# Performance work log

Measured on AMD Instinct MI355X. Metric: run time of the kernel, lower is better.

Reference implementation:

```python
import jax, jax.numpy as jnp
import numpy as np

N_NODES = 50000  # 4 node types x 12500
N_PER = 12500
E = 600000
H = 128
IN_DIMS = [128, 128, 64, 64]


def setup_inputs() -> dict:
    key = jax.random.key(0)
    ks = jax.random.split(key, 16)
    inp = {}
    for i, d in enumerate(IN_DIMS):
        inp[f"feat{i}"] = jax.random.normal(ks[i], (N_PER, d), dtype=jnp.float32)
        # xavier_normal-ish init, gain 1.414
        std = 1.414 * np.sqrt(2.0 / (d + H))
        inp[f"W_fc{i}"] = jax.random.normal(ks[4 + i], (d, H), dtype=jnp.float32) * std
        inp[f"b_fc{i}"] = jnp.zeros((H,), dtype=jnp.float32)
    inp["src"] = jax.random.randint(ks[8], (E,), 0, N_NODES, dtype=jnp.int32)
    inp["dst"] = jax.random.randint(ks[9], (E,), 0, N_NODES, dtype=jnp.int32)
    inp["e_feat"] = jax.random.randint(ks[10], (E,), 0, 36, dtype=jnp.int32)
    inp["b_g0"] = jnp.zeros((H,), dtype=jnp.float32)  # GraphConv layer0 (weight=False, bias)
    inp["W_g1"] = jax.random.normal(ks[11], (H, H), dtype=jnp.float32) * np.sqrt(1.0 / H)
    inp["b_g1"] = jnp.zeros((H,), dtype=jnp.float32)
    return inp


def _degree_norms(src, dst):
    ones = jnp.ones((src.shape[0],), dtype=jnp.float32)
    deg_out = jax.ops.segment_sum(ones, src, num_segments=N_NODES)
    deg_in = jax.ops.segment_sum(ones, dst, num_segments=N_NODES)
    # DGL norm='both': D_out^{-1/2} on src side, D_in^{-1/2} on dst side (clamp 0-degree)
    out_norm = jax.lax.rsqrt(jnp.maximum(deg_out, 1.0))
    in_norm = jax.lax.rsqrt(jnp.maximum(deg_in, 1.0))
    return out_norm, in_norm


def _gcn_aggregate(h, src, dst, out_norm, in_norm):
    m = (h * out_norm[:, None])[src]                      # [E, H] gather
    agg = jax.ops.segment_sum(m, dst, num_segments=N_NODES)
    return agg * in_norm[:, None]


def reference(feat0, feat1, feat2, feat3,
              W_fc0, b_fc0, W_fc1, b_fc1, W_fc2, b_fc2, W_fc3, b_fc3,
              src, dst, e_feat, b_g0, W_g1, b_g1):
    # per-node-type linear projections, then concat along node dim
    h = jnp.concatenate([
        feat0 @ W_fc0 + b_fc0,
        feat1 @ W_fc1 + b_fc1,
        feat2 @ W_fc2 + b_fc2,
        feat3 @ W_fc3 + b_fc3,
    ], axis=0)  # [N_NODES, H]

    out_norm, in_norm = _degree_norms(src, dst)
    # GraphConv layer 0: weight=False, bias, activation (dropout p=0 -> identity)
    h = jax.nn.relu(_gcn_aggregate(h, src, dst, out_norm, in_norm) + b_g0)
    # GraphConv layer 1: aggregate, then linear weight + bias, activation
    h = jax.nn.relu(_gcn_aggregate(h, src, dst, out_norm, in_norm) @ W_g1 + b_g1)

    e = e_feat.astype(jnp.float32)  # e_feat.reshape(-1,1).float() in original
    # forward graph: msg = ft + sum_{r in 0..4} where(e==r, ft, 0) = ft * (1 + 1{e in 0..4})
    w_fwd = 1.0 + sum((e == float(r)).astype(jnp.float32) for r in (0, 1, 2, 3, 4))
    agg_a = jax.ops.segment_sum(h[src] * w_fwd[:, None], dst, num_segments=N_NODES)
    # transpose graph (reversed edges, same e): msg = sum_{r in {6,14,30}} where(e==r, ft, 0)
    w_bwd = sum((e == float(r)).astype(jnp.float32) for r in (6, 14, 30))
    agg_b = jax.ops.segment_sum(h[dst] * w_bwd[:, None], src, num_segments=N_NODES)
    return agg_a + agg_b
```

## Files before the change

### kernel.cpp

```cpp
#include <hip/hip_runtime.h>
#include <hip/hip_bf16.h>

#define N_NODES 50000
#define N_PER   12500
#define E_EDGES 600000
#define HDIM    128

#define NBLK_FC    ((N_PER + 63) / 64)
#define NBLK_NODE  ((N_NODES + 255) / 256)
#define MASK31  0x7fffffff

#define HQD 64
#define HSL_D (E_EDGES / HQD)
#define NBLK_DB (HQD * 4)
#define HQS 32
#define HSL_S (E_EDGES / HQS)
#define NBLK_S (HQS * 4)

typedef __attribute__((ext_vector_type(8))) short bfrag;
typedef __attribute__((ext_vector_type(4))) float ffrag;

__device__ __forceinline__ unsigned short f2bf(float f) {
    union { float f; unsigned u; } x; x.f = f;
    unsigned r = x.u + 0x7fffu + ((x.u >> 16) & 1u);
    return (unsigned short)(r >> 16);
}
__device__ __forceinline__ float lo_bf(unsigned v) { return __uint_as_float(v << 16); }
__device__ __forceinline__ float hi_bf(unsigned v) { return __uint_as_float(v & 0xffff0000u); }
__device__ __forceinline__ unsigned pack2(float a, float b) {
    return (unsigned)f2bf(a) | ((unsigned)f2bf(b) << 16);
}
__device__ __forceinline__ float onrm_of(int deg) {
    return rsqrtf(fmaxf((float)deg, 1.0f));
}

__device__ __forceinline__ void acc8_add(float* acc, uint4 v) {
    acc[0] += lo_bf(v.x); acc[1] += hi_bf(v.x);
    acc[2] += lo_bf(v.y); acc[3] += hi_bf(v.y);
    acc[4] += lo_bf(v.z); acc[5] += hi_bf(v.z);
    acc[6] += lo_bf(v.w); acc[7] += hi_bf(v.w);
}
__device__ __forceinline__ void acc8_addw(float* acc, uint4 v, float w) {
    acc[0] += lo_bf(v.x) * w; acc[1] += hi_bf(v.x) * w;
    acc[2] += lo_bf(v.y) * w; acc[3] += hi_bf(v.y) * w;
    acc[4] += lo_bf(v.z) * w; acc[5] += hi_bf(v.z) * w;
    acc[6] += lo_bf(v.w) * w; acc[7] += hi_bf(v.w) * w;
}

__global__ __launch_bounds__(256) void prep_kernel(
    const float* __restrict__ W0, const float* __restrict__ W1,
    const float* __restrict__ W2, const float* __restrict__ W3,
    const float* __restrict__ Wg,
    const int* __restrict__ src, const int* __restrict__ dst,
    const int* __restrict__ ef,
    unsigned short* __restrict__ Wp,
    unsigned short* __restrict__ partialS,
    unsigned short* __restrict__ partialD,
    unsigned char*  __restrict__ partialB) {
    __shared__ unsigned hist[N_PER];
    int b = blockIdx.x;
    if (b < NBLK_DB) {
        const int q = b >> 2;
        const int p = b & 3;
        const int g0 = p * N_PER;
        for (int j = threadIdx.x; j < N_PER; j += 256) hist[j] = 0;
        __syncthreads();
        const int e0 = q * HSL_D;
        for (int i = e0 + threadIdx.x; i < e0 + HSL_D; i += 256) {
            int d = dst[i], t = ef[i], s = src[i];
            unsigned rd = (unsigned)(d - g0);
            if (rd < (unsigned)N_PER) atomicAdd(&hist[rd], 1u);
            if (t == 6 || t == 14 || t == 30) {
                unsigned rs = (unsigned)(s - g0);
                if (rs < (unsigned)N_PER) atomicAdd(&hist[rs], 0x10000u);
            }
        }
        __syncthreads();
        for (int j = threadIdx.x; j < N_PER; j += 256) {
            unsigned h = hist[j];
            partialD[(size_t)q * N_NODES + g0 + j] = (unsigned short)(h & 0xffffu);
            partialB[(size_t)q * N_NODES + g0 + j] = (unsigned char)(h >> 16);
        }
    } else if (b < NBLK_DB + NBLK_S) {
        const int r = b - NBLK_DB;
        const int q = r >> 2;
        const int p = r & 3;
        const int g0 = p * N_PER;
        for (int j = threadIdx.x; j < N_PER; j += 256) hist[j] = 0;
        __syncthreads();
        const int e0 = q * HSL_S;
        for (int i = e0 + threadIdx.x; i < e0 + HSL_S; i += 256) {
            unsigned rr = (unsigned)(src[i] - g0);
            if (rr < (unsigned)N_PER) atomicAdd(&hist[rr], 1u);
        }
        __syncthreads();
        for (int j = threadIdx.x; j < N_PER; j += 256)
            partialS[(size_t)q * N_NODES + g0 + j] = (unsigned short)hist[j];
    } else {
        int tid = (b - (NBLK_DB + NBLK_S)) * 256 + threadIdx.x;
        const float* W; int D, base, off;
        if      (tid < 2048) { W = W0; D = 128; base = 0;    off = 0;     }
        else if (tid < 4096) { W = W1; D = 128; base = 2048; off = 16384; }
        else if (tid < 5120) { W = W2; D = 64;  base = 4096; off = 32768; }
        else if (tid < 6144) { W = W3; D = 64;  base = 5120; off = 40960; }
        else                 { W = Wg; D = 128; base = 6144; off = 49152; }
        int t2 = tid - base;
        int KT = D / 32;
        int l = t2 & 63;
        int tt = t2 >> 6;
        int kt = tt % KT, n0 = tt / KT;
        int n = n0 * 16 + (l & 15);
        int kb = kt * 32 + (l >> 4) * 8;
#pragma unroll
        for (int j = 0; j < 8; ++j)
            Wp[(size_t)off + (size_t)t2 * 8 + j] = f2bf(W[(size_t)(kb + j) * 128 + n]);
    }
}

__global__ __launch_bounds__(256) void plane_prefix_kernel(
    unsigned short* __restrict__ partialD, unsigned char* __restrict__ partialB,
    int* __restrict__ degD, int* __restrict__ degB,
    int* __restrict__ scanD, int* __restrict__ scanB,
    int* __restrict__ blocksumD, int* __restrict__ blocksumB) {
    const int t = threadIdx.x;
    const int n = blockIdx.x * 256 + t;
    int dD = 0, dB = 0;
    if (n < N_NODES) {
        int run = 0;
#pragma unroll
        for (int q = 0; q < HQD; ++q) {
            size_t ix = (size_t)q * N_NODES + n;
            int c = partialD[ix];
            partialD[ix] = (unsigned short)run;
            run += c;
        }
        dD = run; degD[n] = run;
        run = 0;
#pragma unroll
        for (int q = 0; q < HQD; ++q) {
            size_t ix = (size_t)q * N_NODES + n;
            int c = partialB[ix];
            partialB[ix] = (unsigned char)run;
            run += c;
        }
        dB = run; degB[n] = run;
    }
    __shared__ int sD[256], sB[256];
    sD[t] = dD; sB[t] = dB;
    __syncthreads();
    for (int off = 1; off < 256; off <<= 1) {
        int xD = (t >= off) ? sD[t - off] : 0;
        int xB = (t >= off) ? sB[t - off] : 0;
        __syncthreads();
        sD[t] += xD; sB[t] += xB;
        __syncthreads();
    }
    if (n < N_NODES) {
        scanD[n] = sD[t] - dD;
        scanB[n] = sB[t] - dB;
    }
    if (t == 255) {
        blocksumD[blockIdx.x] = sD[255];
        blocksumB[blockIdx.x] = sB[255];
    }
}

__global__ __launch_bounds__(256) void base_add_kernel(
    const int* __restrict__ blocksumD, const int* __restrict__ blocksumB,
    int* __restrict__ scanD, int* __restrict__ scanB) {
    __shared__ int sD[256], sB[256];
    const int t = threadIdx.x;
    const int bid = blockIdx.x;
    sD[t] = (t < bid) ? blocksumD[t] : 0;
    sB[t] = (t < bid) ? blocksumB[t] : 0;
    __syncthreads();
    for (int off = 128; off >= 1; off >>= 1) {
        if (t < off) { sD[t] += sD[t + off]; sB[t] += sB[t + off]; }
        __syncthreads();
    }
    const int n = bid * 256 + t;
    if (n < N_NODES) { scanD[n] += sD[0]; scanB[n] += sB[0]; }
}

__global__ __launch_bounds__(1024) void scatter_kernel(
    const int* __restrict__ src, const int* __restrict__ dst,
    const int* __restrict__ ef,
    const unsigned short* __restrict__ prefD,
    const unsigned char*  __restrict__ prefB,
    const int* __restrict__ scanD, const int* __restrict__ scanB,
    int* __restrict__ bucket, int* __restrict__ bucketB)
{
    __shared__ unsigned offP[N_PER];
    const int b = blockIdx.x;
    const int q = b >> 2;
    const int p = b & 3;
    const int g0 = p * N_PER;
    for (int j = threadIdx.x; j < N_PER; j += 1024)
        offP[j] = (unsigned)(scanD[g0 + j] + (int)prefD[(size_t)q * N_NODES + g0 + j])
                | ((unsigned)prefB[(size_t)q * N_NODES + g0 + j] << 20);
    __syncthreads();
    const int e0 = q * HSL_D;
    for (int i = e0 + threadIdx.x; i < e0 + HSL_D; i += 1024) {
        int s = src[i], d = dst[i], t = ef[i];
        unsigned rd = (unsigned)(d - g0);
        if (rd < (unsigned)N_PER) {
            unsigned old = atomicAdd(&offP[rd], 1u);
            bucket[old & 0xFFFFFu] = s | ((t <= 4) ? 0x80000000 : 0);
        }
        if (t == 6 || t == 14 || t == 30) {
            unsigned rs = (unsigned)(s - g0);
            if (rs < (unsigned)N_PER) {
                unsigned old = atomicAdd(&offP[rs], 1u << 20);
                bucketB[scanB[s] + (int)(old >> 20)] = d;
            }
        }
    }
}

template<int D>
__device__ __forceinline__ void fc_body(
    int blk, int tid,
    const float* __restrict__ X,
    const unsigned short* __restrict__ Wp,
    const float* __restrict__ bias,
    unsigned short* __restrict__ outbf,
    int rows)
{
    constexpr int KT = D / 32;
    const int lane = tid & 63;
    const int wave = tid >> 6;
    const int m = lane & 15, q = lane >> 4;
    const int rbase = blk * 64 + wave * 16;
    const int row = rbase + m;

    bfrag afr[KT];
#pragma unroll
    for (int kt = 0; kt < KT; ++kt) {
        bfrag a;
        if (row < rows) {
            const float* xp = X + (size_t)row * D + kt * 32 + q * 8;
            float4 u0 = *(const float4*)xp;
            float4 u1 = *(const float4*)(xp + 4);
            a[0] = (short)f2bf(u0.x); a[1] = (short)f2bf(u0.y);
            a[2] = (short)f2bf(u0.z); a[3] = (short)f2bf(u0.w);
            a[4] = (short)f2bf(u1.x); a[5] = (short)f2bf(u1.y);
            a[6] = (short)f2bf(u1.z); a[7] = (short)f2bf(u1.w);
        } else {
#pragma unroll
            for (int t = 0; t < 8; ++t) a[t] = 0;
        }
        afr[kt] = a;
    }

    ffrag acc[8];
#pragma unroll
    for (int n0 = 0; n0 < 8; ++n0)
#pragma unroll
        for (int t = 0; t < 4; ++t) acc[n0][t] = 0.f;

#pragma unroll
    for (int n0 = 0; n0 < 8; ++n0)
#pragma unroll
        for (int kt = 0; kt < KT; ++kt) {
            bfrag bfr = *(const bfrag*)(Wp + ((size_t)(n0 * KT + kt) * 64 + lane) * 8);
            acc[n0] = __builtin_amdgcn_mfma_f32_16x16x32_bf16(afr[kt], bfr, acc[n0], 0, 0, 0);
        }

#pragma unroll
    for (int n0 = 0; n0 < 8; ++n0) {
        const int col = n0 * 16 + m;
        const float bj = bias[col];
#pragma unroll
        for (int r = 0; r < 4; ++r) {
            int orow = rbase + q * 4 + r;
            if (orow < rows)
                outbf[(size_t)orow * 128 + col] = f2bf(acc[n0][r] + bj);
        }
    }
}

__global__ __launch_bounds__(256) void fc_kernel(
    const float* __restrict__ f0, const float* __restrict__ f1,
    const float* __restrict__ f2, const float* __restrict__ f3,
    const unsigned short* __restrict__ Wp,
    const float* __restrict__ b0, const float* __restrict__ b1,
    const float* __restrict__ b2, const float* __restrict__ b3,
    unsigned short* __restrict__ Abf)
{
    int fb = blockIdx.x;
    int which = fb / NBLK_FC;
    int blk = fb - which * NBLK_FC;
    if (which == 0)
        fc_body<128>(blk, threadIdx.x, f0, Wp,         b0, Abf + (size_t)0 * N_PER * HDIM, N_PER);
    else if (which == 1)
        fc_body<128>(blk, threadIdx.x, f1, Wp + 16384, b1, Abf + (size_t)1 * N_PER * HDIM, N_PER);
    else if (which == 2)
        fc_body<64>(blk, threadIdx.x, f2, Wp + 32768, b2, Abf + (size_t)2 * N_PER * HDIM, N_PER);
    else
        fc_body<64>(blk, threadIdx.x, f3, Wp + 40960, b3, Abf + (size_t)3 * N_PER * HDIM, N_PER);
}

__global__ __launch_bounds__(256) void scale_kernel(
    uint4* __restrict__ A, const unsigned short* __restrict__ partialS,
    float* __restrict__ onrm_buf) {
    int idx = blockIdx.x * blockDim.x + threadIdx.x;
    int n = idx >> 4, j8 = idx & 15;
    int d = (int)partialS[(size_t)j8 * N_NODES + n]
          + (int)partialS[(size_t)(j8 + 16) * N_NODES + n];
    d += __shfl_xor(d, 1);
    d += __shfl_xor(d, 2);
    d += __shfl_xor(d, 4);
    d += __shfl_xor(d, 8);
    float on = onrm_of(d);
    if (j8 == 0) onrm_buf[n] = on;
    uint4 v = A[(size_t)n * 16 + j8];
    uint4 o;
    o.x = pack2(lo_bf(v.x) * on, hi_bf(v.x) * on);
    o.y = pack2(lo_bf(v.y) * on, hi_bf(v.y) * on);
    o.z = pack2(lo_bf(v.z) * on, hi_bf(v.z) * on);
    o.w = pack2(lo_bf(v.w) * on, hi_bf(v.w) * on);
    A[(size_t)n * 16 + j8] = o;
}

__global__ __launch_bounds__(256) void agg0_kernel(
    const uint4* __restrict__ A,
    const int* __restrict__ bucket, const int* __restrict__ scanD,
    const int* __restrict__ degD,
    const float* __restrict__ onrm_buf, const float* __restrict__ b_g0,
    uint4* __restrict__ B) {
    int idx = blockIdx.x * blockDim.x + threadIdx.x;
    int n = idx >> 4, j8 = idx & 15;
    const int cnt = degD[n];
    const int* bk = bucket + scanD[n];
    float acc[8] = {0.f, 0.f, 0.f, 0.f, 0.f, 0.f, 0.f, 0.f};
    int i = 0;
    for (; i + 4 <= cnt; i += 4) {
        int s0 = bk[i] & MASK31,     s1 = bk[i + 1] & MASK31;
        int s2 = bk[i + 2] & MASK31, s3 = bk[i + 3] & MASK31;
        uint4 v0 = A[(size_t)s0 * 16 + j8];
        uint4 v1 = A[(size_t)s1 * 16 + j8];
        uint4 v2 = A[(size_t)s2 * 16 + j8];
        uint4 v3 = A[(size_t)s3 * 16 + j8];
        acc8_add(acc, v0); acc8_add(acc, v1);
        acc8_add(acc, v2); acc8_add(acc, v3);
    }
    for (; i < cnt; ++i) {
        int s = bk[i] & MASK31;
        acc8_add(acc, A[(size_t)s * 16 + j8]);
    }
    float inr = onrm_of(cnt);
    float onr = onrm_buf[n];
    const float* bg = b_g0 + j8 * 8;
    float r[8];
#pragma unroll
    for (int k = 0; k < 8; ++k)
        r[k] = fmaxf(acc[k] * inr + bg[k], 0.f) * onr;
    uint4 o;
    o.x = pack2(r[0], r[1]); o.y = pack2(r[2], r[3]);
    o.z = pack2(r[4], r[5]); o.w = pack2(r[6], r[7]);
    B[(size_t)n * 16 + j8] = o;
}

__global__ __launch_bounds__(256) void gemm1_fused_kernel(
    const unsigned short* __restrict__ Bbf,
    const int* __restrict__ bucket, const int* __restrict__ scanD,
    const int* __restrict__ degD,
    const unsigned short* __restrict__ Wp, const float* __restrict__ bias,
    unsigned short* __restrict__ outbf)
{
    const int lane = threadIdx.x & 63;
    const int wave = threadIdx.x >> 6;
    const int m = lane & 15, q = lane >> 4;
    const int rbase = blockIdx.x * 64 + wave * 16;
    const int node = rbase + m;

    float ga[32];
#pragma unroll
    for (int i = 0; i < 32; ++i) ga[i] = 0.f;

    if (node < N_NODES) {
        const int cnt = degD[node];
        const int* bk = bucket + scanD[node];
        int i = 0;
        for (; i + 2 <= cnt; i += 2) {
            int s0 = bk[i] & MASK31, s1 = bk[i + 1] & MASK31;
            const uint4* r0 = (const uint4*)(Bbf + (size_t)s0 * 128);
            const uint4* r1 = (const uint4*)(Bbf + (size_t)s1 * 128);
            uint4 a0 = r0[0 * 4 + q], a1 = r0[1 * 4 + q], a2 = r0[2 * 4 + q], a3 = r0[3 * 4 + q];
            uint4 c0 = r1[0 * 4 + q], c1 = r1[1 * 4 + q], c2 = r1[2 * 4 + q], c3 = r1[3 * 4 + q];
            acc8_add(ga +  0, a0); acc8_add(ga +  8, a1);
            acc8_add(ga + 16, a2); acc8_add(ga + 24, a3);
            acc8_add(ga +  0, c0); acc8_add(ga +  8, c1);
            acc8_add(ga + 16, c2); acc8_add(ga + 24, c3);
        }
        for (; i < cnt; ++i) {
            int s = bk[i] & MASK31;
            const uint4* rp = (const uint4*)(Bbf + (size_t)s * 128);
#pragma unroll
            for (int kt = 0; kt < 4; ++kt) acc8_add(ga + kt * 8, rp[kt * 4 + q]);
        }
    }

    bfrag afr[4];
#pragma unroll
    for (int kt = 0; kt < 4; ++kt)
#pragma unroll
        for (int j = 0; j < 8; ++j)
            afr[kt][j] = (short)f2bf(ga[kt * 8 + j]);

    ffrag acc[8];
#pragma unroll
    for (int n0 = 0; n0 < 8; ++n0)
#pragma unroll
        for (int t = 0; t < 4; ++t) acc[n0][t] = 0.f;

#pragma unroll
    for (int n0 = 0; n0 < 8; ++n0)
#pragma unroll
        for (int kt = 0; kt < 4; ++kt) {
            bfrag bfr = *(const bfrag*)(Wp + ((size_t)(n0 * 4 + kt) * 64 + lane) * 8);
            acc[n0] = __builtin_amdgcn_mfma_f32_16x16x32_bf16(afr[kt], bfr, acc[n0], 0, 0, 0);
        }

    float ir[4];
#pragma unroll
    for (int r = 0; r < 4; ++r) {
        int orow = rbase + q * 4 + r;
        ir[r] = (orow < N_NODES) ? onrm_of(degD[orow]) : 0.f;
    }
#pragma unroll
    for (int n0 = 0; n0 < 8; ++n0) {
        const int col = n0 * 16 + m;
        const float bj = bias[col];
#pragma unroll
        for (int r = 0; r < 4; ++r) {
            int orow = rbase + q * 4 + r;
            if (orow < N_NODES)
                outbf[(size_t)orow * 128 + col] = f2bf(fmaxf(acc[n0][r] * ir[r] + bj, 0.f));
        }
    }
}

__global__ __launch_bounds__(256) void final_kernel(
    const uint4* __restrict__ H,
    const int* __restrict__ bucket, const int* __restrict__ scanD,
    const int* __restrict__ degD,
    const int* __restrict__ bucketB, const int* __restrict__ scanB,
    const int* __restrict__ degB,
    float4* __restrict__ out4) {
    int idx = blockIdx.x * blockDim.x + threadIdx.x;
    int n = idx >> 4, j8 = idx & 15;
    float acc[8] = {0.f, 0.f, 0.f, 0.f, 0.f, 0.f, 0.f, 0.f};
    const int cnt = degD[n];
    const int* bk = bucket + scanD[n];
    int i = 0;
    for (; i + 4 <= cnt; i += 4) {
        int c0 = bk[i], c1 = bk[i + 1], c2 = bk[i + 2], c3 = bk[i + 3];
        uint4 v0 = H[(size_t)(c0 & MASK31) * 16 + j8];
        uint4 v1 = H[(size_t)(c1 & MASK31) * 16 + j8];
        uint4 v2 = H[(size_t)(c2 & MASK31) * 16 + j8];
        uint4 v3 = H[(size_t)(c3 & MASK31) * 16 + j8];
        acc8_addw(acc, v0, (c0 < 0) ? 2.0f : 1.0f);
        acc8_addw(acc, v1, (c1 < 0) ? 2.0f : 1.0f);
        acc8_addw(acc, v2, (c2 < 0) ? 2.0f : 1.0f);
        acc8_addw(acc, v3, (c3 < 0) ? 2.0f : 1.0f);
    }
    for (; i < cnt; ++i) {
        int c = bk[i];
        acc8_addw(acc, H[(size_t)(c & MASK31) * 16 + j8], (c < 0) ? 2.0f : 1.0f);
    }
    const int cb = degB[n];
    const int* bkB = bucketB + scanB[n];
    for (int k = 0; k < cb; ++k) {
        int d = bkB[k];
        acc8_add(acc, H[(size_t)d * 16 + j8]);
    }
    float4 o0 = {acc[0], acc[1], acc[2], acc[3]};
    float4 o1 = {acc[4], acc[5], acc[6], acc[7]};
    out4[(size_t)n * 32 + j8 * 2]     = o0;
    out4[(size_t)n * 32 + j8 * 2 + 1] = o1;
}

extern "C" void kernel_launch(void* const* d_in, const int* in_sizes, int n_in,
                              void* d_out, int out_size, void* d_ws, size_t ws_size,
                              hipStream_t stream) {
    const float* feat[4]  = {(const float*)d_in[0], (const float*)d_in[3],
                             (const float*)d_in[6], (const float*)d_in[9]};
    const float* W_fc[4]  = {(const float*)d_in[1], (const float*)d_in[4],
                             (const float*)d_in[7], (const float*)d_in[10]};
    const float* b_fc[4]  = {(const float*)d_in[2], (const float*)d_in[5],
                             (const float*)d_in[8], (const float*)d_in[11]};
    const int*   src      = (const int*)d_in[12];
    const int*   dst      = (const int*)d_in[13];
    const int*   efeat    = (const int*)d_in[14];
    const float* b_g0     = (const float*)d_in[15];
    const float* W_g1     = (const float*)d_in[16];
    const float* b_g1     = (const float*)d_in[17];
    float* out = (float*)d_out;

    char* p = (char*)d_ws;
    unsigned short* Abf = (unsigned short*)p; p += (size_t)N_NODES * HDIM * 2;
    unsigned short* Bbf = (unsigned short*)p; p += (size_t)N_NODES * HDIM * 2;
    unsigned short* Wp  = (unsigned short*)p; p += (size_t)65536 * 2;
    int* bucket  = (int*)p; p += (size_t)E_EDGES * 4;
    int* bucketB = (int*)p; p += (size_t)E_EDGES * 4;
    unsigned short* partialS = (unsigned short*)p; p += (size_t)HQS * N_NODES * 2;
    unsigned short* partialD = (unsigned short*)p; p += (size_t)HQD * N_NODES * 2;
    unsigned char*  partialB = (unsigned char*)p;  p += (size_t)HQD * N_NODES;
    int* degD  = (int*)p; p += (size_t)N_NODES * 4;
    int* degB  = (int*)p; p += (size_t)N_NODES * 4;
    int* scanD = (int*)p; p += (size_t)N_NODES * 4;
    int* scanB = (int*)p; p += (size_t)N_NODES * 4;
    float* onrm_buf = (float*)p; p += (size_t)N_NODES * 4;
    int* blocksumD = (int*)p; p += 256 * 4;
    int* blocksumB = (int*)p; p += 256 * 4;

    const unsigned short* Wpg = Wp + 49152;

    prep_kernel<<<NBLK_DB + NBLK_S + 32, 256, 0, stream>>>(
        W_fc[0], W_fc[1], W_fc[2], W_fc[3], W_g1, src, dst, efeat,
        Wp, partialS, partialD, partialB);

    plane_prefix_kernel<<<NBLK_NODE, 256, 0, stream>>>(
        partialD, partialB, degD, degB, scanD, scanB, blocksumD, blocksumB);

    base_add_kernel<<<NBLK_NODE, 256, 0, stream>>>(
        blocksumD, blocksumB, scanD, scanB);

    scatter_kernel<<<NBLK_DB, 1024, 0, stream>>>(
        src, dst, efeat, partialD, partialB, scanD, scanB, bucket, bucketB);

    fc_kernel<<<4 * NBLK_FC, 256, 0, stream>>>(
        feat[0], feat[1], feat[2], feat[3], Wp,
        b_fc[0], b_fc[1], b_fc[2], b_fc[3], Abf);

    const int grid_node = (N_NODES * 16) / 256;

    scale_kernel<<<grid_node, 256, 0, stream>>>((uint4*)Abf, partialS, onrm_buf);

    agg0_kernel<<<grid_node, 256, 0, stream>>>(
        (const uint4*)Abf, bucket, scanD, degD, onrm_buf, b_g0, (uint4*)Bbf);

    gemm1_fused_kernel<<<(N_NODES + 63) / 64, 256, 0, stream>>>(
        Bbf, bucket, scanD, degD, Wpg, b_g1, Abf);

    final_kernel<<<grid_node, 256, 0, stream>>>(
        (const uint4*)Abf, bucket, scanD, degD, bucketB, scanB, degB, (float4*)out);
}
```

Measured before the change: 274.9 us.

## Apply W_g1 before layer-1 aggregation and fold out-norm scaling into FC epilogue

```diff
diff --git a/kernel.cpp b/kernel.cpp
--- a/kernel.cpp
+++ b/kernel.cpp
@@ -7,6 +7,7 @@
 #define HDIM    128
 
 #define NBLK_FC    ((N_PER + 63) / 64)
+#define NBLK_G     ((N_NODES + 63) / 64)
 #define NBLK_NODE  ((N_NODES + 255) / 256)
 #define MASK31  0x7fffffff
 
@@ -119,9 +120,11 @@
 
 __global__ __launch_bounds__(256) void plane_prefix_kernel(
     unsigned short* __restrict__ partialD, unsigned char* __restrict__ partialB,
+    const unsigned short* __restrict__ partialS,
     int* __restrict__ degD, int* __restrict__ degB,
     int* __restrict__ scanD, int* __restrict__ scanB,
-    int* __restrict__ blocksumD, int* __restrict__ blocksumB) {
+    int* __restrict__ blocksumD, int* __restrict__ blocksumB,
+    float* __restrict__ onrm_buf) {
     const int t = threadIdx.x;
     const int n = blockIdx.x * 256 + t;
     int dD = 0, dB = 0;
@@ -144,6 +147,11 @@
             run += c;
         }
         dB = run; degB[n] = run;
+        int dS = 0;
+#pragma unroll
+        for (int q = 0; q < HQS; ++q)
+            dS += partialS[(size_t)q * N_NODES + n];
+        onrm_buf[n] = onrm_of(dS);
     }
     __shared__ int sD[256], sB[256];
     sD[t] = dD; sB[t] = dB;
@@ -223,6 +231,7 @@
     const float* __restrict__ X,
     const unsigned short* __restrict__ Wp,
     const float* __restrict__ bias,
+    const float* __restrict__ onrm,
     unsigned short* __restrict__ outbf,
     int rows)
 {
@@ -274,7 +283,8 @@
         for (int r = 0; r < 4; ++r) {
             int orow = rbase + q * 4 + r;
             if (orow < rows)
-                outbf[(size_t)orow * 128 + col] = f2bf(acc[n0][r] + bj);
+                outbf[(size_t)orow * 128 + col] =
+                    f2bf((acc[n0][r] + bj) * onrm[orow]);
         }
     }
 }
@@ -285,41 +295,24 @@
     const unsigned short* __restrict__ Wp,
     const float* __restrict__ b0, const float* __restrict__ b1,
     const float* __restrict__ b2, const float* __restrict__ b3,
+    const float* __restrict__ onrm_buf,
     unsigned short* __restrict__ Abf)
 {
     int fb = blockIdx.x;
     int which = fb / NBLK_FC;
     int blk = fb - which * NBLK_FC;
     if (which == 0)
-        fc_body<128>(blk, threadIdx.x, f0, Wp,         b0, Abf + (size_t)0 * N_PER * HDIM, N_PER);
+        fc_body<128>(blk, threadIdx.x, f0, Wp,         b0, onrm_buf,
+                     Abf + (size_t)0 * N_PER * HDIM, N_PER);
     else if (which == 1)
-        fc_body<128>(blk, threadIdx.x, f1, Wp + 16384, b1, Abf + (size_t)1 * N_PER * HDIM, N_PER);
+        fc_body<128>(blk, threadIdx.x, f1, Wp + 16384, b1, onrm_buf + N_PER,
+                     Abf + (size_t)1 * N_PER * HDIM, N_PER);
     else if (which == 2)
-        fc_body<64>(blk, threadIdx.x, f2, Wp + 32768, b2, Abf + (size_t)2 * N_PER * HDIM, N_PER);
+        fc_body<64>(blk, threadIdx.x, f2, Wp + 32768, b2, onrm_buf + 2 * N_PER,
+                    Abf + (size_t)2 * N_PER * HDIM, N_PER);
     else
-        fc_body<64>(blk, threadIdx.x, f3, Wp + 40960, b3, Abf + (size_t)3 * N_PER * HDIM, N_PER);
-}
-
-__global__ __launch_bounds__(256) void scale_kernel(
-    uint4* __restrict__ A, const unsigned short* __restrict__ partialS,
-    float* __restrict__ onrm_buf) {
-    int idx = blockIdx.x * blockDim.x + threadIdx.x;
-    int n = idx >> 4, j8 = idx & 15;
-    int d = (int)partialS[(size_t)j8 * N_NODES + n]
-          + (int)partialS[(size_t)(j8 + 16) * N_NODES + n];
-    d += __shfl_xor(d, 1);
-    d += __shfl_xor(d, 2);
-    d += __shfl_xor(d, 4);
-    d += __shfl_xor(d, 8);
-    float on = onrm_of(d);
-    if (j8 == 0) onrm_buf[n] = on;
-    uint4 v = A[(size_t)n * 16 + j8];
-    uint4 o;
-    o.x = pack2(lo_bf(v.x) * on, hi_bf(v.x) * on);
-    o.y = pack2(lo_bf(v.y) * on, hi_bf(v.y) * on);
-    o.z = pack2(lo_bf(v.z) * on, hi_bf(v.z) * on);
-    o.w = pack2(lo_bf(v.w) * on, hi_bf(v.w) * on);
-    A[(size_t)n * 16 + j8] = o;
+        fc_body<64>(blk, threadIdx.x, f3, Wp + 40960, b3, onrm_buf + 3 * N_PER,
+                    Abf + (size_t)3 * N_PER * HDIM, N_PER);
 }
 
 __global__ __launch_bounds__(256) void agg0_kernel(
@@ -361,52 +354,27 @@
     B[(size_t)n * 16 + j8] = o;
 }
 
-__global__ __launch_bounds__(256) void gemm1_fused_kernel(
+__global__ __launch_bounds__(256) void gemmg_kernel(
     const unsigned short* __restrict__ Bbf,
-    const int* __restrict__ bucket, const int* __restrict__ scanD,
-    const int* __restrict__ degD,
-    const unsigned short* __restrict__ Wp, const float* __restrict__ bias,
-    unsigned short* __restrict__ outbf)
+    const unsigned short* __restrict__ Wp,
+    unsigned short* __restrict__ BWbf)
 {
     const int lane = threadIdx.x & 63;
     const int wave = threadIdx.x >> 6;
     const int m = lane & 15, q = lane >> 4;
     const int rbase = blockIdx.x * 64 + wave * 16;
-    const int node = rbase + m;
-
-    float ga[32];
-#pragma unroll
-    for (int i = 0; i < 32; ++i) ga[i] = 0.f;
-
-    if (node < N_NODES) {
-        const int cnt = degD[node];
-        const int* bk = bucket + scanD[node];
-        int i = 0;
-        for (; i + 2 <= cnt; i += 2) {
-            int s0 = bk[i] & MASK31, s1 = bk[i + 1] & MASK31;
-            const uint4* r0 = (const uint4*)(Bbf + (size_t)s0 * 128);
-            const uint4* r1 = (const uint4*)(Bbf + (size_t)s1 * 128);
-            uint4 a0 = r0[0 * 4 + q], a1 = r0[1 * 4 + q], a2 = r0[2 * 4 + q], a3 = r0[3 * 4 + q];
-            uint4 c0 = r1[0 * 4 + q], c1 = r1[1 * 4 + q], c2 = r1[2 * 4 + q], c3 = r1[3 * 4 + q];
-            acc8_add(ga +  0, a0); acc8_add(ga +  8, a1);
-            acc8_add(ga + 16, a2); acc8_add(ga + 24, a3);
-            acc8_add(ga +  0, c0); acc8_add(ga +  8, c1);
-            acc8_add(ga + 16, c2); acc8_add(ga + 24, c3);
-        }
-        for (; i < cnt; ++i) {
-            int s = bk[i] & MASK31;
-            const uint4* rp = (const uint4*)(Bbf + (size_t)s * 128);
-#pragma unroll
-            for (int kt = 0; kt < 4; ++kt) acc8_add(ga + kt * 8, rp[kt * 4 + q]);
-        }
-    }
+    const int row = rbase + m;
 
     bfrag afr[4];
 #pragma unroll
-    for (int kt = 0; kt < 4; ++kt)
-#pragma unroll
-        for (int j = 0; j < 8; ++j)
-            afr[kt][j] = (short)f2bf(ga[kt * 8 + j]);
+    for (int kt = 0; kt < 4; ++kt) {
+        if (row < N_NODES)
+            afr[kt] = *(const bfrag*)(Bbf + (size_t)row * 128 + kt * 32 + q * 8);
+        else {
+#pragma unroll
+            for (int t = 0; t < 8; ++t) afr[kt][t] = 0;
+        }
+    }
 
     ffrag acc[8];
 #pragma unroll
@@ -422,23 +390,54 @@
             acc[n0] = __builtin_amdgcn_mfma_f32_16x16x32_bf16(afr[kt], bfr, acc[n0], 0, 0, 0);
         }
 
-    float ir[4];
-#pragma unroll
-    for (int r = 0; r < 4; ++r) {
-        int orow = rbase + q * 4 + r;
-        ir[r] = (orow < N_NODES) ? onrm_of(degD[orow]) : 0.f;
-    }
 #pragma unroll
     for (int n0 = 0; n0 < 8; ++n0) {
         const int col = n0 * 16 + m;
-        const float bj = bias[col];
 #pragma unroll
         for (int r = 0; r < 4; ++r) {
             int orow = rbase + q * 4 + r;
             if (orow < N_NODES)
-                outbf[(size_t)orow * 128 + col] = f2bf(fmaxf(acc[n0][r] * ir[r] + bj, 0.f));
-        }
-    }
+                BWbf[(size_t)orow * 128 + col] = f2bf(acc[n0][r]);
+        }
+    }
+}
+
+__global__ __launch_bounds__(256) void agg1_kernel(
+    const uint4* __restrict__ BW,
+    const int* __restrict__ bucket, const int* __restrict__ scanD,
+    const int* __restrict__ degD,
+    const float* __restrict__ b_g1,
+    uint4* __restrict__ H) {
+    int idx = blockIdx.x * blockDim.x + threadIdx.x;
+    int n = idx >> 4, j8 = idx & 15;
+    const int cnt = degD[n];
+    const int* bk = bucket + scanD[n];
+    float acc[8] = {0.f, 0.f, 0.f, 0.f, 0.f, 0.f, 0.f, 0.f};
+    int i = 0;
+    for (; i + 4 <= cnt; i += 4) {
+        int s0 = bk[i] & MASK31,     s1 = bk[i + 1] & MASK31;
+        int s2 = bk[i + 2] & MASK31, s3 = bk[i + 3] & MASK31;
+        uint4 v0 = BW[(size_t)s0 * 16 + j8];
+        uint4 v1 = BW[(size_t)s1 * 16 + j8];
+        uint4 v2 = BW[(size_t)s2 * 16 + j8];
+        uint4 v3 = BW[(size_t)s3 * 16 + j8];
+        acc8_add(acc, v0); acc8_add(acc, v1);
+        acc8_add(acc, v2); acc8_add(acc, v3);
+    }
+    for (; i < cnt; ++i) {
+        int s = bk[i] & MASK31;
+        acc8_add(acc, BW[(size_t)s * 16 + j8]);
+    }
+    float inr = onrm_of(cnt);
+    const float* bg = b_g1 + j8 * 8;
+    float r[8];
+#pragma unroll
+    for (int k = 0; k < 8; ++k)
+        r[k] = fmaxf(acc[k] * inr + bg[k], 0.f);
+    uint4 o;
+    o.x = pack2(r[0], r[1]); o.y = pack2(r[2], r[3]);
+    o.z = pack2(r[4], r[5]); o.w = pack2(r[6], r[7]);
+    H[(size_t)n * 16 + j8] = o;
 }
 
 __global__ __launch_bounds__(256) void final_kernel(
@@ -522,7 +521,8 @@
         Wp, partialS, partialD, partialB);
 
     plane_prefix_kernel<<<NBLK_NODE, 256, 0, stream>>>(
-        partialD, partialB, degD, degB, scanD, scanB, blocksumD, blocksumB);
+        partialD, partialB, partialS, degD, degB, scanD, scanB,
+        blocksumD, blocksumB, onrm_buf);
 
     base_add_kernel<<<NBLK_NODE, 256, 0, stream>>>(
         blocksumD, blocksumB, scanD, scanB);
@@ -532,18 +532,18 @@
 
     fc_kernel<<<4 * NBLK_FC, 256, 0, stream>>>(
         feat[0], feat[1], feat[2], feat[3], Wp,
-        b_fc[0], b_fc[1], b_fc[2], b_fc[3], Abf);
+        b_fc[0], b_fc[1], b_fc[2], b_fc[3], onrm_buf, Abf);
 
     const int grid_node = (N_NODES * 16) / 256;
-
-    scale_kernel<<<grid_node, 256, 0, stream>>>((uint4*)Abf, partialS, onrm_buf);
 
     agg0_kernel<<<grid_node, 256, 0, stream>>>(
         (const uint4*)Abf, bucket, scanD, degD, onrm_buf, b_g0, (uint4*)Bbf);
 
-    gemm1_fused_kernel<<<(N_NODES + 63) / 64, 256, 0, stream>>>(
-        Bbf, bucket, scanD, degD, Wpg, b_g1, Abf);
+    gemmg_kernel<<<NBLK_G, 256, 0, stream>>>(Bbf, Wpg, Abf);
+
+    agg1_kernel<<<grid_node, 256, 0, stream>>>(
+        (const uint4*)Abf, bucket, scanD, degD, b_g1, (uint4*)Bbf);
 
     final_kernel<<<grid_node, 256, 0, stream>>>(
-        (const uint4*)Abf, bucket, scanD, degD, bucketB, scanB, degB, (float4*)out);
-}
+        (const uint4*)Bbf, bucket, scanD, degD, bucketB, scanB, degB, (float4*)out);
+}
```

Result: faster. 258.8 us (-5.9%).
